# Kernel optimization log

Hardware: AMD Instinct MI355X
Metric: run time of the kernel (lower is better)

Reference implementation:

```python
import jax, jax.numpy as jnp
import numpy as np

SHAPES = ((64, 64), (32, 32), (16, 16), (8, 8))
HEADS, LV, P = 8, 4, 8


def _ln(x, g, b, eps=1e-5):
    m = x.mean(-1, keepdims=True)
    v = ((x - m) ** 2).mean(-1, keepdims=True)
    return (x - m) * jax.lax.rsqrt(v + eps) * g + b


def _sample_level(v, H, W, loc):
    # v: [B, heads, H*W, hd] value for one level; loc: [B, L, heads, P, 2] in [0,1]
    # Matches F.grid_sample(mode='bilinear', padding_mode='zeros', align_corners=False)
    x = loc[..., 0] * W - 0.5
    y = loc[..., 1] * H - 0.5
    x0 = jnp.floor(x)
    y0 = jnp.floor(y)
    B, L, hds, Pn = x.shape
    acc = 0.0
    for dx, dy in ((0, 0), (1, 0), (0, 1), (1, 1)):
        xi = x0 + dx
        yi = y0 + dy
        w = (1.0 - jnp.abs(x - xi)) * (1.0 - jnp.abs(y - yi))
        valid = (xi >= 0) & (xi < W) & (yi >= 0) & (yi < H)
        idx = (jnp.clip(yi, 0, H - 1) * W + jnp.clip(xi, 0, W - 1)).astype(jnp.int32)
        idx_r = idx.transpose(0, 2, 1, 3).reshape(B, hds, L * Pn)  # [B,heads,L*P]
        g = jnp.take_along_axis(v, idx_r[..., None], axis=2)  # [B,heads,L*P,hd]
        g = g.reshape(B, hds, L, Pn, -1).transpose(0, 2, 1, 3, 4)  # [B,L,heads,P,hd]
        acc = acc + (w * valid.astype(w.dtype))[..., None] * g
    return acc


def setup_inputs() -> dict:
    key = jax.random.key(0)
    ks = iter(jax.random.split(key, 64))
    B, d, depth, dff = 2, 256, 6, 1024
    inp = {}
    for i, (H, W) in enumerate(SHAPES):
        inp[f"src{i}"] = jax.random.normal(next(ks), (B, d, H, W), jnp.float32)
        inp[f"pos{i}"] = jax.random.normal(next(ks), (B, d, H, W), jnp.float32)
    s = 0.02
    off_dim = HEADS * LV * P * 2  # 512
    aw_dim = HEADS * LV * P  # 256
    inp["level_embed"] = jax.random.normal(next(ks), (LV, d), jnp.float32)
    inp["W_off"] = jax.random.normal(next(ks), (depth, d, off_dim), jnp.float32) * s
    inp["b_off"] = jax.random.normal(next(ks), (depth, off_dim), jnp.float32) * 0.5
    inp["W_attn"] = jax.random.normal(next(ks), (depth, d, aw_dim), jnp.float32) * s
    inp["b_attn"] = jnp.zeros((depth, aw_dim), jnp.float32)
    inp["W_val"] = jax.random.normal(next(ks), (depth, d, d), jnp.float32) * s
    inp["b_val"] = jnp.zeros((depth, d), jnp.float32)
    inp["W_out"] = jax.random.normal(next(ks), (depth, d, d), jnp.float32) * s
    inp["b_out"] = jnp.zeros((depth, d), jnp.float32)
    inp["ln1_g"] = jnp.ones((depth, d), jnp.float32)
    inp["ln1_b"] = jnp.zeros((depth, d), jnp.float32)
    inp["W1"] = jax.random.normal(next(ks), (depth, d, dff), jnp.float32) * s
    inp["b1"] = jnp.zeros((depth, dff), jnp.float32)
    inp["W2"] = jax.random.normal(next(ks), (depth, dff, d), jnp.float32) * s
    inp["b2"] = jnp.zeros((depth, d), jnp.float32)
    inp["ln2_g"] = jnp.ones((depth, d), jnp.float32)
    inp["ln2_b"] = jnp.zeros((depth, d), jnp.float32)
    return inp


def reference(src0, src1, src2, src3, pos0, pos1, pos2, pos3, level_embed,
              W_off, b_off, W_attn, b_attn, W_val, b_val, W_out, b_out,
              ln1_g, ln1_b, W1, b1, W2, b2, ln2_g, ln2_b):
    srcs = [src0, src1, src2, src3]
    poss = [pos0, pos1, pos2, pos3]
    B, d = src0.shape[0], src0.shape[1]
    hd = d // HEADS
    # flatten multi-scale maps: [B, C, H, W] -> [B, H*W, C]
    src_flat = jnp.concatenate([s.reshape(B, d, -1).transpose(0, 2, 1) for s in srcs], 1)
    pos_flat = jnp.concatenate(
        [p.reshape(B, d, -1).transpose(0, 2, 1) + level_embed[i] for i, p in enumerate(poss)], 1)
    # reference points; masks are all-False so valid_ratios == 1 (same ref for every level)
    refs = []
    for (H, W) in SHAPES:
        gy, gx = jnp.meshgrid((jnp.arange(H) + 0.5) / H, (jnp.arange(W) + 0.5) / W, indexing='ij')
        refs.append(jnp.stack([gx.reshape(-1), gy.reshape(-1)], -1))
    ref = jnp.concatenate(refs, 0)  # [L, 2]
    norm = jnp.array([[W, H] for (H, W) in SHAPES], jnp.float32)  # [LV, 2] (W_, H_)
    sizes = [H * W for (H, W) in SHAPES]
    starts = np.cumsum([0] + sizes[:-1]).tolist()
    depth = W_off.shape[0]
    L = src_flat.shape[1]
    x = src_flat
    for i in range(depth):
        # pre-norm deformable self-attention; value comes from un-normed residual stream
        x2 = _ln(x, ln1_g[i], ln1_b[i])
        q = x2 + pos_flat
        off = (q @ W_off[i] + b_off[i]).reshape(B, L, HEADS, LV, P, 2)
        attn = jax.nn.softmax((q @ W_attn[i] + b_attn[i]).reshape(B, L, HEADS, LV * P), -1)
        attn = attn.reshape(B, L, HEADS, LV, P)
        val = (x @ W_val[i] + b_val[i]).reshape(B, L, HEADS, hd).transpose(0, 2, 1, 3)  # [B,heads,L,hd]
        loc = ref[None, :, None, None, None, :] + off / norm[None, None, None, :, None, :]
        out = 0.0
        for l, (H, W) in enumerate(SHAPES):
            vl = val[:, :, starts[l]:starts[l] + sizes[l]]
            sl = _sample_level(vl, H, W, loc[:, :, :, l])  # [B,L,heads,P,hd]
            out = out + (attn[:, :, :, l, :, None] * sl).sum(3)
        out = out.reshape(B, L, d) @ W_out[i] + b_out[i]
        x = x + out
        # pre-norm FFN with exact gelu (torch default)
        x2 = _ln(x, ln2_g[i], ln2_b[i])
        x = x + jax.nn.gelu(x2 @ W1[i] + b1[i], approximate=False) @ W2[i] + b2[i]
    return x
```

## Files before the change

### kernel.cpp

```cpp
#include <hip/hip_runtime.h>
#include <hip/hip_bf16.h>
#include <math.h>

#define L_TOK 5440
#define NTOK  10880
#define D     256

typedef __attribute__((ext_vector_type(8))) short short8;
typedef __attribute__((ext_vector_type(4))) short short4v;
typedef __attribute__((ext_vector_type(4))) float f32x4;
typedef __attribute__((ext_vector_type(2))) float v2f;
typedef __attribute__((ext_vector_type(4))) int int4v;

__device__ __forceinline__ short f2bf(float f) {
    __hip_bfloat16 h = __float2bfloat16(f);
    return __builtin_bit_cast(short, h);
}
__device__ __forceinline__ float bf2f(short s) {
    unsigned u = ((unsigned)(unsigned short)s) << 16;
    return __builtin_bit_cast(float, u);
}

#define GLL16(gp, lp) \
    __builtin_amdgcn_global_load_lds((const __attribute__((address_space(1))) void*)(gp), \
                                     (__attribute__((address_space(3))) void*)(lp), 16, 0, 0)

__global__ __launch_bounds__(256) void flat_all(
    const float* __restrict__ s0, const float* __restrict__ p0,
    const float* __restrict__ s1, const float* __restrict__ p1,
    const float* __restrict__ s2, const float* __restrict__ p2,
    const float* __restrict__ s3, const float* __restrict__ p3,
    const float* __restrict__ le,
    float* __restrict__ x, short* __restrict__ xb, float* __restrict__ pos)
{
    __shared__ float ts[32][33], tp[32][33];
    int idx = blockIdx.x;
    const float *s, *p; int HW, start, lv, xt;
    if (idx < 2048)      {             s = s0; p = p0; HW = 4096; start = 0;    lv = 0; xt = 128; }
    else if (idx < 2560) { idx -= 2048; s = s1; p = p1; HW = 1024; start = 4096; lv = 1; xt = 32; }
    else if (idx < 2688) { idx -= 2560; s = s2; p = p2; HW = 256;  start = 5120; lv = 2; xt = 8; }
    else                 { idx -= 2688; s = s3; p = p3; HW = 64;   start = 5376; lv = 3; xt = 2; }
    int pix0 = (idx % xt) * 32;
    int rem  = idx / xt;
    int c0   = (rem & 7) * 32;
    int b    = rem >> 3;
    int tx = threadIdx.x & 31, ty = threadIdx.x >> 5;
#pragma unroll
    for (int i = 0; i < 4; ++i) {
        int c = c0 + ty + i * 8;
        size_t gi = ((size_t)b * D + c) * HW + pix0 + tx;
        ts[ty + i * 8][tx] = s[gi];
        tp[ty + i * 8][tx] = p[gi];
    }
    __syncthreads();
#pragma unroll
    for (int i = 0; i < 4; ++i) {
        int pix = pix0 + ty + i * 8;
        size_t bl = (size_t)b * L_TOK + start + pix;
        int c = c0 + tx;
        float v = ts[tx][ty + i * 8];
        x[bl * D + c]   = v;
        xb[bl * D + c]  = f2bf(v);
        pos[bl * D + c] = tp[tx][ty + i * 8] + le[lv * D + c];
    }
}

__global__ __launch_bounds__(256) void wconv_all(
    const float* __restrict__ Woff, const float* __restrict__ Watt,
    const float* __restrict__ Wval, const float* __restrict__ Wout,
    const float* __restrict__ W1,   const float* __restrict__ W2,
    const float* __restrict__ boff, const float* __restrict__ batt,
    short* __restrict__ wt_qa, short* __restrict__ wt_val, short* __restrict__ wt_out,
    short* __restrict__ wt_1,  short* __restrict__ wt_2, float* __restrict__ bqa)
{
    __shared__ float tile[32][33];
    int tidx = blockIdx.x, d = blockIdx.z;
    if (tidx == 832) {
        for (int c = threadIdx.x; c < 768; c += 256)
            bqa[d * 768 + c] = (c < 512) ? boff[d * 512 + c] : batt[d * 256 + c - 512];
        return;
    }
    const float* W; short* Wt; int K, N, dstride, rowoff, nx, t;
    if (tidx < 128)      { W = Woff; Wt = wt_qa;  K = 256;  N = 512;  dstride = 768 * 256;  rowoff = 0;   nx = 16; t = tidx; }
    else if (tidx < 192) { W = Watt; Wt = wt_qa;  K = 256;  N = 256;  dstride = 768 * 256;  rowoff = 512; nx = 8;  t = tidx - 128; }
    else if (tidx < 256) { W = Wval; Wt = wt_val; K = 256;  N = 256;  dstride = 256 * 256;  rowoff = 0;   nx = 8;  t = tidx - 192; }
    else if (tidx < 320) { W = Wout; Wt = wt_out; K = 256;  N = 256;  dstride = 256 * 256;  rowoff = 0;   nx = 8;  t = tidx - 256; }
    else if (tidx < 576) { W = W1;   Wt = wt_1;   K = 256;  N = 1024; dstride = 1024 * 256; rowoff = 0;   nx = 32; t = tidx - 320; }
    else                 { W = W2;   Wt = wt_2;   K = 1024; N = 256;  dstride = 256 * 1024; rowoff = 0;   nx = 8;  t = tidx - 576; }
    int n0 = (t % nx) * 32, k0 = (t / nx) * 32;
    const float* Wd = W + (size_t)d * K * N;
    short* Wtd = Wt + (size_t)d * dstride + (size_t)rowoff * K;
    int tx = threadIdx.x & 31, ty = threadIdx.x >> 5;
#pragma unroll
    for (int i = 0; i < 4; ++i)
        tile[ty + i * 8][tx] = Wd[(size_t)(k0 + ty + i * 8) * N + n0 + tx];
    __syncthreads();
#pragma unroll
    for (int i = 0; i < 4; ++i)
        Wtd[(size_t)(n0 + ty + i * 8) * K + k0 + tx] = f2bf(tile[tx][ty + i * 8]);
}

__global__ __launch_bounds__(256) void ln_kernel(
    const float* __restrict__ x, const float* __restrict__ g, const float* __restrict__ bta,
    const float* __restrict__ pos, short* __restrict__ out)
{
    int wid = threadIdx.x >> 6, lane = threadIdx.x & 63;
    int m = blockIdx.x * 4 + wid;
    int c4 = lane * 4;
    const float4 xv = *(const float4*)&x[(size_t)m * D + c4];
    float s = xv.x + xv.y + xv.z + xv.w;
#pragma unroll
    for (int o = 32; o; o >>= 1) s += __shfl_xor(s, o);
    float mean = s * (1.0f / D);
    float d0 = xv.x - mean, d1 = xv.y - mean, d2 = xv.z - mean, d3 = xv.w - mean;
    float sq = d0 * d0 + d1 * d1 + d2 * d2 + d3 * d3;
#pragma unroll
    for (int o = 32; o; o >>= 1) sq += __shfl_xor(sq, o);
    float rstd = rsqrtf(sq * (1.0f / D) + 1e-5f);
    const float4 gv = *(const float4*)&g[c4];
    const float4 bv = *(const float4*)&bta[c4];
    float o0 = d0 * rstd * gv.x + bv.x;
    float o1 = d1 * rstd * gv.y + bv.y;
    float o2 = d2 * rstd * gv.z + bv.z;
    float o3 = d3 * rstd * gv.w + bv.w;
    if (pos) {
        const float4 pv = *(const float4*)&pos[(size_t)m * D + c4];
        o0 += pv.x; o1 += pv.y; o2 += pv.z; o3 += pv.w;
    }
    short4v ov;
    ov[0] = f2bf(o0); ov[1] = f2bf(o1); ov[2] = f2bf(o2); ov[3] = f2bf(o3);
    *(short4v*)&out[(size_t)m * D + c4] = ov;
}

template<int BN>
__device__ __forceinline__ void mm_body64(
    const short* __restrict__ A, const short* __restrict__ Wt,
    const float* __restrict__ bias, const float* __restrict__ resid,
    float* __restrict__ Cf, short* __restrict__ Cb,
    int row0, int col0, int K, int ldc, int act, int f16out)
{
    constexpr int NW  = BN / 4;
    constexpr int NF  = NW / 16;
    constexpr int BCH = BN / 32;
    __shared__ __align__(16) short As[2][64 * 64];
    __shared__ __align__(16) short Bs[2][BN * 64];
    int tid = threadIdx.x, lane = tid & 63, w = tid >> 6;
    int l15 = lane & 15, l16 = lane >> 4;

    int a_off[4][2], b_off[NF][2];
#pragma unroll
    for (int m = 0; m < 4; ++m)
#pragma unroll
        for (int kk = 0; kk < 2; ++kk) {
            int ra = m * 16 + l15;
            a_off[m][kk] = ra * 64 + (((kk * 4 + l16) ^ (ra & 7)) << 3);
        }
#pragma unroll
    for (int n = 0; n < NF; ++n)
#pragma unroll
        for (int kk = 0; kk < 2; ++kk) {
            int rb = w * NW + n * 16 + l15;
            b_off[n][kk] = rb * 64 + (((kk * 4 + l16) ^ (rb & 7)) << 3);
        }

    int sg = (lane & 7) ^ ((lane >> 3) & 7);
    const short* ag = A  + (size_t)(row0 + w * 16 + (lane >> 3)) * K + sg * 8;
    const short* bg = Wt + (size_t)(col0 + w * NW + (lane >> 3)) * K + sg * 8;

    f32x4 acc[4][NF];
#pragma unroll
    for (int m = 0; m < 4; ++m)
#pragma unroll
        for (int n = 0; n < NF; ++n) acc[m][n] = (f32x4){0.f, 0.f, 0.f, 0.f};

    auto stage = [&](int buf, int kofs) {
#pragma unroll
        for (int c = 0; c < 2; ++c)
            GLL16(ag + (size_t)c * 8 * K + kofs, &As[buf][w * 1024 + c * 512]);
#pragma unroll
        for (int c = 0; c < BCH; ++c)
            GLL16(bg + (size_t)c * 8 * K + kofs, &Bs[buf][w * NW * 64 + c * 512]);
    };
    auto comp = [&](int buf) {
#pragma unroll
        for (int kk = 0; kk < 2; ++kk) {
            short8 af[4], bfr[NF];
#pragma unroll
            for (int m = 0; m < 4; ++m) af[m] = *(short8*)&As[buf][a_off[m][kk]];
#pragma unroll
            for (int n = 0; n < NF; ++n) bfr[n] = *(short8*)&Bs[buf][b_off[n][kk]];
#pragma unroll
            for (int m = 0; m < 4; ++m)
#pragma unroll
                for (int n = 0; n < NF; ++n)
                    acc[m][n] = __builtin_amdgcn_mfma_f32_16x16x32_bf16(af[m], bfr[n], acc[m][n], 0, 0, 0);
        }
    };

    stage(0, 0);
    __syncthreads();
    int cur = 0;
    for (int k0 = 64; k0 < K; k0 += 64) {
        stage(cur ^ 1, k0);
        comp(cur);
        __syncthreads();
        cur ^= 1;
    }
    comp(cur);

#pragma unroll
    for (int m = 0; m < 4; ++m) {
#pragma unroll
        for (int j = 0; j < 4; ++j) {
            int row = row0 + m * 16 + l16 * 4 + j;
#pragma unroll
            for (int n = 0; n < NF; ++n) {
                int col = col0 + w * NW + n * 16 + l15;
                float v = acc[m][n][j] + bias[col];
                if (act) v = 0.5f * v * (1.0f + erff(v * 0.70710678118654752f));
                if (resid) v += resid[(size_t)row * ldc + col];
                if (Cf) Cf[(size_t)row * ldc + col] = v;
                if (Cb) Cb[(size_t)row * ldc + col] =
                    f16out ? __builtin_bit_cast(short, (_Float16)v) : f2bf(v);
            }
        }
    }
}

template<int BN>
__global__ __launch_bounds__(256) void mm_kernel(
    const short* __restrict__ A, const short* __restrict__ Wt,
    const float* __restrict__ bias, const float* __restrict__ resid,
    float* __restrict__ Cf, short* __restrict__ Cb, int K, int ldc, int act)
{
    mm_body64<BN>(A, Wt, bias, resid, Cf, Cb, blockIdx.y * 64, blockIdx.x * BN, K, ldc, act, 0);
}

__global__ __launch_bounds__(256) void mm2_kernel(
    const short* __restrict__ A1, const short* __restrict__ Wt1, const float* __restrict__ bias1,
    short* __restrict__ C1, int ldc1,
    const short* __restrict__ A2, const short* __restrict__ Wt2, const float* __restrict__ bias2,
    short* __restrict__ C2, int ldc2,
    int nx1, int K)
{
    const short *A, *Wt; const float* bias; short* Cb; int ldc, col0, f16o;
    if ((int)blockIdx.x < nx1) {
        A = A1; Wt = Wt1; bias = bias1; Cb = C1; ldc = ldc1; f16o = 1;
        col0 = blockIdx.x * 128;
    } else {
        A = A2; Wt = Wt2; bias = bias2; Cb = C2; ldc = ldc2; f16o = 0;
        col0 = (blockIdx.x - nx1) * 128;
    }
    mm_body64<128>(A, Wt, bias, nullptr, nullptr, Cb, blockIdx.y * 64, col0, K, ldc, 0, f16o);
}

__global__ __launch_bounds__(256) void sample_kernel(
    const short* __restrict__ big, const short* __restrict__ val, short* __restrict__ out)
{
    __shared__ float sw[8 * 132];
    __shared__ int   si[8 * 132];
    __shared__ _Float16 rowl[768];
    int bl = blockIdx.x;
    int b = bl / L_TOK, l = bl - b * L_TOK;
    const _Float16* row = (const _Float16*)big + (size_t)bl * 768;
    int t = threadIdx.x;
    if (t < 96) *(int4v*)&rowl[t * 8] = *(const int4v*)&row[t * 8];
    __syncthreads();
    {
        int head = t >> 5, lvp = t & 31, lv = lvp >> 3, p = lvp & 7;
        int lq, r;
        if (l < 4096)      { lq = 0; r = l;        }
        else if (l < 5120) { lq = 1; r = l - 4096; }
        else if (l < 5376) { lq = 2; r = l - 5120; }
        else               { lq = 3; r = l - 5376; }
        int sh = 6 - lq;
        float invSq = 1.0f / (float)(1 << sh);
        float refx = ((r & ((1 << sh) - 1)) + 0.5f) * invSq;
        float refy = ((r >> sh) + 0.5f) * invSq;
        int S = 64 >> lv;
        int start = (lv == 0) ? 0 : (lv == 1) ? 4096 : (lv == 2) ? 5120 : 5376;
        float Sf = (float)S;
        float logit = (float)rowl[512 + head * 32 + lvp];
        float mx = logit;
#pragma unroll
        for (int o = 16; o; o >>= 1) mx = fmaxf(mx, __shfl_xor(mx, o));
        float e = __expf(logit - mx);
        float ssum = e;
#pragma unroll
        for (int o = 16; o; o >>= 1) ssum += __shfl_xor(ssum, o);
        float a = e / ssum;
        float ox = (float)rowl[head * 64 + lv * 16 + p * 2 + 0];
        float oy = (float)rowl[head * 64 + lv * 16 + p * 2 + 1];
        float X = refx * Sf + ox - 0.5f;
        float Y = refy * Sf + oy - 0.5f;
        float x0 = floorf(X), y0 = floorf(Y);
        float fx = X - x0, fy = Y - y0;
        int xi0 = (int)x0, yi0 = (int)y0;
        int qt = lvp >> 3, sidx = lvp & 7;
        int base_w = head * 132 + qt * 33 + sidx * 4;
#pragma unroll
        for (int tap = 0; tap < 4; ++tap) {
            int dx = tap & 1, dy = tap >> 1;
            int xi = xi0 + dx, yi = yi0 + dy;
            float wgt = (dx ? fx : 1.0f - fx) * (dy ? fy : 1.0f - fy);
            bool valid = (xi >= 0) && (xi < S) && (yi >= 0) && (yi < S);
            int xc = xi < 0 ? 0 : (xi > S - 1 ? S - 1 : xi);
            int yc = yi < 0 ? 0 : (yi > S - 1 ? S - 1 : yi);
            sw[base_w + tap] = valid ? wgt * a : 0.0f;
            si[base_w + tap] = (start + yc * S + xc) << 8;
        }
    }
    __syncthreads();
    int h = t >> 5, sgp = (t >> 2) & 7, cg = t & 3;
    const short* vb = val + (size_t)b * L_TOK * D + h * 32 + cg * 8;
    v2f A0 = {0.f, 0.f}, A1 = {0.f, 0.f}, A2 = {0.f, 0.f}, A3 = {0.f, 0.f};
#pragma unroll
    for (int gp = 0; gp < 2; ++gp) {
        float w8[8]; int i8[8];
#pragma unroll
        for (int ss = 0; ss < 2; ++ss) {
            int base = h * 132 + (gp * 2 + ss) * 33 + sgp * 4;
#pragma unroll
            for (int tap = 0; tap < 4; ++tap) {
                w8[ss * 4 + tap] = sw[base + tap];
                i8[ss * 4 + tap] = si[base + tap];
            }
        }
        int4v gv[8];
#pragma unroll
        for (int k = 0; k < 8; ++k) gv[k] = *(const int4v*)&vb[i8[k]];
#pragma unroll
        for (int k = 0; k < 8; ++k) {
            v2f wp = {w8[k], w8[k]};
#pragma unroll
            for (int q = 0; q < 4; ++q) {
                unsigned dq = (unsigned)gv[k][q];
                v2f vv;
                vv[0] = __builtin_bit_cast(float, dq << 16);
                vv[1] = __builtin_bit_cast(float, dq & 0xffff0000u);
                if (q == 0) asm("v_pk_fma_f32 %0, %1, %2, %0" : "+v"(A0) : "v"(wp), "v"(vv));
                if (q == 1) asm("v_pk_fma_f32 %0, %1, %2, %0" : "+v"(A1) : "v"(wp), "v"(vv));
                if (q == 2) asm("v_pk_fma_f32 %0, %1, %2, %0" : "+v"(A2) : "v"(wp), "v"(vv));
                if (q == 3) asm("v_pk_fma_f32 %0, %1, %2, %0" : "+v"(A3) : "v"(wp), "v"(vv));
            }
        }
    }
    float r0 = A0[0], r1 = A0[1], r2 = A1[0], r3 = A1[1];
    float r4 = A2[0], r5 = A2[1], r6 = A3[0], r7 = A3[1];
#pragma unroll
    for (int o = 4; o <= 16; o <<= 1) {
        r0 += __shfl_xor(r0, o); r1 += __shfl_xor(r1, o);
        r2 += __shfl_xor(r2, o); r3 += __shfl_xor(r3, o);
        r4 += __shfl_xor(r4, o); r5 += __shfl_xor(r5, o);
        r6 += __shfl_xor(r6, o); r7 += __shfl_xor(r7, o);
    }
    if (sgp == 0) {
        short8 o;
        o[0] = f2bf(r0); o[1] = f2bf(r1); o[2] = f2bf(r2); o[3] = f2bf(r3);
        o[4] = f2bf(r4); o[5] = f2bf(r5); o[6] = f2bf(r6); o[7] = f2bf(r7);
        *(short8*)&out[(size_t)bl * D + h * 32 + cg * 8] = o;
    }
}

extern "C" void kernel_launch(void* const* d_in, const int* in_sizes, int n_in,
                              void* d_out, int out_size, void* d_ws, size_t ws_size,
                              hipStream_t stream)
{
    const float* s0    = (const float*)d_in[0];
    const float* p0    = (const float*)d_in[1];
    const float* s1    = (const float*)d_in[2];
    const float* p1    = (const float*)d_in[3];
    const float* s2    = (const float*)d_in[4];
    const float* p2    = (const float*)d_in[5];
    const float* s3    = (const float*)d_in[6];
    const float* p3    = (const float*)d_in[7];
    const float* lvl   = (const float*)d_in[8];
    const float* W_off = (const float*)d_in[9];
    const float* b_off = (const float*)d_in[10];
    const float* W_att = (const float*)d_in[11];
    const float* b_att = (const float*)d_in[12];
    const float* W_val = (const float*)d_in[13];
    const float* b_val = (const float*)d_in[14];
    const float* W_out = (const float*)d_in[15];
    const float* b_out = (const float*)d_in[16];
    const float* ln1g  = (const float*)d_in[17];
    const float* ln1b  = (const float*)d_in[18];
    const float* W1    = (const float*)d_in[19];
    const float* b1    = (const float*)d_in[20];
    const float* W2    = (const float*)d_in[21];
    const float* b2    = (const float*)d_in[22];
    const float* ln2g  = (const float*)d_in[23];
    const float* ln2b  = (const float*)d_in[24];

    const size_t S1 = (size_t)NTOK * D;
    float* xbuf = (float*)d_ws;
    float* pos  = xbuf + S1;
    float* bigf = pos + S1;
    float* bqa  = bigf + 3 * S1;
    short* big  = (short*)bigf;
    short* qbf   = (short*)(bqa + 6 * 768);
    short* x_bf  = qbf + S1;
    short* valbf = x_bf + S1;
    short* sampb = valbf + S1;
    short* hidbf = sampb + S1;
    short* wt_qa  = hidbf + 4 * S1;
    short* wt_val = wt_qa  + (size_t)6 * 768 * 256;
    short* wt_out = wt_val + (size_t)6 * 256 * 256;
    short* wt_1   = wt_out + (size_t)6 * 256 * 256;
    short* wt_2   = wt_1   + (size_t)6 * 1024 * 256;

    wconv_all<<<dim3(833, 1, 6), 256, 0, stream>>>(
        W_off, W_att, W_val, W_out, W1, W2, b_off, b_att,
        wt_qa, wt_val, wt_out, wt_1, wt_2, bqa);

    flat_all<<<2720, 256, 0, stream>>>(s0, p0, s1, p1, s2, p2, s3, p3, lvl, xbuf, x_bf, pos);

    for (int i = 0; i < 6; ++i) {
        ln_kernel<<<NTOK / 4, 256, 0, stream>>>(xbuf, ln1g + i * 256, ln1b + i * 256, pos, qbf);
        mm2_kernel<<<dim3(8, 170), 256, 0, stream>>>(
            qbf, wt_qa + (size_t)i * 768 * 256, bqa + i * 768, big, 768,
            x_bf, wt_val + (size_t)i * 256 * 256, b_val + i * 256, valbf, 256,
            6, 256);
        sample_kernel<<<NTOK, 256, 0, stream>>>(big, valbf, sampb);
        mm_kernel<64><<<dim3(4, 170), 256, 0, stream>>>(
            sampb, wt_out + (size_t)i * 256 * 256, b_out + i * 256, xbuf, xbuf, nullptr, 256, 256, 0);
        ln_kernel<<<NTOK / 4, 256, 0, stream>>>(xbuf, ln2g + i * 256, ln2b + i * 256, nullptr, qbf);
        mm_kernel<128><<<dim3(8, 170), 256, 0, stream>>>(
            qbf, wt_1 + (size_t)i * 1024 * 256, b1 + i * 1024, nullptr, nullptr, hidbf, 256, 1024, 1);
        float* outp = (i == 5) ? (float*)d_out : xbuf;
        short* xbp  = (i == 5) ? nullptr : x_bf;
        mm_kernel<64><<<dim3(4, 170), 256, 0, stream>>>(
            hidbf, wt_2 + (size_t)i * 256 * 1024, b2 + i * 256, xbuf, outp, xbp, 1024, 256, 0);
    }
}
```

Baseline: 746.5 us.

## Triple-buffer GEMM LDS staging with explicit vmcnt waits

Converts the bf16 MFMA GEMM body from a double-buffered LDS pipeline with __syncthreads to a three-stage ring of A/B tiles. Explicit s_waitcnt vmcnt counts let two tile loads stay in flight while the current tile is computed, so global-to-LDS latency is hidden better. The cost is 50% more LDS per block, which may lower occupancy. Correctness depends on the vmcnt constants matching the number of async loads each stage issues per wave.

```diff
diff --git a/kernel.cpp b/kernel.cpp
--- a/kernel.cpp
+++ b/kernel.cpp
@@ -24,6 +24,15 @@
 #define GLL16(gp, lp) \
     __builtin_amdgcn_global_load_lds((const __attribute__((address_space(1))) void*)(gp), \
                                      (__attribute__((address_space(3))) void*)(lp), 16, 0, 0)
+
+template<int N> __device__ __forceinline__ void waitcnt_vm() {
+    if constexpr (N == 0)       asm volatile("s_waitcnt vmcnt(0)" ::: "memory");
+    else if constexpr (N == 4)  asm volatile("s_waitcnt vmcnt(4)" ::: "memory");
+    else if constexpr (N == 6)  asm volatile("s_waitcnt vmcnt(6)" ::: "memory");
+    else if constexpr (N == 8)  asm volatile("s_waitcnt vmcnt(8)" ::: "memory");
+    else if constexpr (N == 12) asm volatile("s_waitcnt vmcnt(12)" ::: "memory");
+    __builtin_amdgcn_sched_barrier(0);
+}
 
 __global__ __launch_bounds__(256) void flat_all(
     const float* __restrict__ s0, const float* __restrict__ p0,
@@ -142,8 +151,9 @@
     constexpr int NW  = BN / 4;
     constexpr int NF  = NW / 16;
     constexpr int BCH = BN / 32;
-    __shared__ __align__(16) short As[2][64 * 64];
-    __shared__ __align__(16) short Bs[2][BN * 64];
+    constexpr int LPW = 2 + BCH;
+    __shared__ __align__(16) short As[3][64 * 64];
+    __shared__ __align__(16) short Bs[3][BN * 64];
     int tid = threadIdx.x, lane = tid & 63, w = tid >> 6;
     int l15 = lane & 15, l16 = lane >> 4;
 
@@ -198,15 +208,22 @@
     };
 
     stage(0, 0);
-    __syncthreads();
-    int cur = 0;
-    for (int k0 = 64; k0 < K; k0 += 64) {
-        stage(cur ^ 1, k0);
-        comp(cur);
-        __syncthreads();
-        cur ^= 1;
-    }
-    comp(cur);
+    stage(1, 64);
+    int ci = 0;
+    for (int k0 = 128; k0 < K; k0 += 64) {
+        stage((ci + 2) % 3, k0);
+        waitcnt_vm<2 * LPW>();
+        __builtin_amdgcn_s_barrier();
+        comp(ci % 3);
+        __builtin_amdgcn_s_barrier();
+        ++ci;
+    }
+    waitcnt_vm<LPW>();
+    __builtin_amdgcn_s_barrier();
+    comp(ci % 3);
+    waitcnt_vm<0>();
+    __builtin_amdgcn_s_barrier();
+    comp((ci + 1) % 3);
 
 #pragma unroll
     for (int m = 0; m < 4; ++m) {
```

Result: slower. 769.9 us (+3.1%).
